# Kernel tuning notes

Hardware: AMD Instinct MI355X
Metric: run time of the kernel (lower is better)

## Reference

```python
import jax, jax.numpy as jnp
import numpy as np

IN_FEATURES = 4096
OUT_FEATURES = 4096
GROUP_SIZE = 128
PACKED_COLS = IN_FEATURES // 8
GROUP_COUNT = IN_FEATURES // GROUP_SIZE


def setup_inputs() -> dict:
    key = jax.random.key(0)
    k1, k2, k3, k4 = jax.random.split(key, 4)
    x = jax.random.normal(k1, (4, 2048, IN_FEATURES), dtype=jnp.float32)
    # packed int4 weights: 8 nibbles per int32 word
    qweight = jax.random.randint(k2, (OUT_FEATURES, PACKED_COLS), jnp.iinfo(jnp.int32).min, jnp.iinfo(jnp.int32).max, dtype=jnp.int32)
    qscale = (jax.random.uniform(k3, (GROUP_COUNT, OUT_FEATURES), dtype=jnp.float32) + 0.5) * 0.01
    qzeros = jax.random.randint(k4, (GROUP_COUNT, OUT_FEATURES), 0, 16, dtype=jnp.int32)
    return {"x": x, "qweight": qweight, "qscale": qscale, "qzeros": qzeros}


def _dequantize(qweight, qscale, qzeros):
    out_f, packed_cols = qweight.shape
    in_f = packed_cols * 8
    shifts = jnp.arange(0, 32, 4, dtype=jnp.int32)  # 8 nibbles per int32
    # (out, packed, 8) -> (out, in)
    w_int = ((qweight[:, :, None] >> shifts) & 15).reshape(out_f, in_f).astype(jnp.float32)
    w_int = w_int[:, :IN_FEATURES]
    gids = jnp.arange(IN_FEATURES, dtype=jnp.int32) // GROUP_SIZE  # (in,)
    scales = qscale[gids].T   # (out, in)
    zeros = qzeros[gids].astype(jnp.float32).T  # (out, in)
    return (w_int - zeros) * scales


def reference(x, qweight, qscale, qzeros):
    w = _dequantize(qweight, qscale, qzeros).astype(jnp.bfloat16)  # compute_dtype
    y = jnp.einsum('bsi,oi->bso', x.astype(jnp.bfloat16), w)
    return y.astype(x.dtype)
```

## Files before the change

### kernel.cpp

```cpp
#include <hip/hip_runtime.h>
#include <hip/hip_bf16.h>

#define IN_F   4096
#define OUT_F  4096
#define PACKED (IN_F / 8)
#define M_DIM  8192
#define N_DIM  OUT_F
#define K_DIM  IN_F

#define BM 256
#define BN 256
#define BK 64
#define NT (K_DIM / BK)
#define NHALF (4 * NT)

typedef __bf16 bf16x8 __attribute__((ext_vector_type(8)));
typedef float  f32x4  __attribute__((ext_vector_type(4)));

#define BAR() asm volatile("s_barrier" ::: "memory")

__global__ __launch_bounds__(256) void dequant_kernel(
    const int* __restrict__ qw, const float* __restrict__ qs,
    const int* __restrict__ qz, __bf16* __restrict__ W)
{
    int t = blockIdx.x * blockDim.x + threadIdx.x;
    if (t >= OUT_F * PACKED) return;
    int o = t >> 9;
    int c = t & (PACKED - 1);
    int g = c >> 4;
    unsigned int q = (unsigned int)qw[t];
    float scale = qs[g * OUT_F + o];
    float zero  = (float)qz[g * OUT_F + o];
    bf16x8 v;
#pragma unroll
    for (int i = 0; i < 8; ++i) {
        float wi = (float)((q >> (4 * i)) & 15u);
        v[i] = (__bf16)((wi - zero) * scale);
    }
    *reinterpret_cast<bf16x8*>(&W[(size_t)t * 8]) = v;
}

__global__ __launch_bounds__(256) void cvt_kernel(
    const float* __restrict__ x, __bf16* __restrict__ xb, int n8)
{
    int t = blockIdx.x * blockDim.x + threadIdx.x;
    if (t >= n8) return;
    const float4* xv = reinterpret_cast<const float4*>(x);
    float4 a = xv[2 * t];
    float4 b = xv[2 * t + 1];
    bf16x8 v;
    v[0] = (__bf16)a.x; v[1] = (__bf16)a.y; v[2] = (__bf16)a.z; v[3] = (__bf16)a.w;
    v[4] = (__bf16)b.x; v[5] = (__bf16)b.y; v[6] = (__bf16)b.z; v[7] = (__bf16)b.w;
    reinterpret_cast<bf16x8*>(xb)[t] = v;
}

__global__ __launch_bounds__(512, 2) void gemm_kernel(
    const __bf16* __restrict__ A, const __bf16* __restrict__ B,
    float* __restrict__ C)
{
    extern __shared__ __bf16 lds[];

    const int tid  = threadIdx.x;
    const int lane = tid & 63;
    const int wave = tid >> 6;
    const int wm   = wave >> 2;
    const int wn   = wave & 3;

    const int bid = blockIdx.x;
    const int swz = (bid & 7) * 64 + (bid >> 3);
    const int nBase = (swz & 15) * BN;
    const int mBase = (swz >> 4) * BM;

    const int lr = lane & 15;
    const int lk = (lane >> 4) * 8;

    auto stage_half = [&](const __bf16* __restrict__ src, __bf16* dstMat,
                          int rowBase, int k0, int hh) {
#pragma unroll
        for (int i = 0; i < 2; ++i) {
            const int st = hh * 16 + i * 8 + wave;
            const int r  = (st >> 1) * 16 + lr;
            const int c  = (st & 1) * 32 + lk;
            __builtin_amdgcn_global_load_lds(
                (const __attribute__((address_space(1))) void*)(src + (size_t)(rowBase + r) * K_DIM + (k0 + c)),
                (__attribute__((address_space(3))) void*)(dstMat + st * 512 + lane * 8), 16, 0, 0);
        }
    };
    auto stage_H = [&](int H) {
        const int t = H >> 2;
        const int h = H & 3;
        __bf16* base = lds + (size_t)(t & 1) * 32768 + (size_t)(h >> 1) * 16384;
        if (h & 2) stage_half(B, base, nBase, t * BK, h & 1);
        else       stage_half(A, base, mBase, t * BK, h & 1);
    };

    f32x4 acc[8][4];
#pragma unroll
    for (int i = 0; i < 8; ++i)
#pragma unroll
        for (int j = 0; j < 4; ++j)
            acc[i][j] = 0.0f;

#pragma unroll
    for (int H = 0; H < 7; ++H) stage_H(H);
    asm volatile("s_waitcnt vmcnt(6)" ::: "memory");
    BAR();

#define LDA(mi, kb) (*(const bf16x8*)(lA + (((wm * 8 + (mi)) * 2 + (kb)) * 512 + lane * 8)))
#define LDB(ni, kb) (*(const bf16x8*)(lB + (((wn * 4 + (ni)) * 2 + (kb)) * 512 + lane * 8)))

    for (int t = 0; t < NT; ++t) {
        const __bf16* lA = lds + (size_t)(t & 1) * 32768;
        const __bf16* lB = lA + 16384;
        const int Hb = 4 * t + 7;
        bf16x8 Af[8][2];
        bf16x8 Bf[2][2];

#pragma unroll
        for (int mi = 0; mi < 4; ++mi) { Af[mi][0] = LDA(mi, 0); Af[mi][1] = LDA(mi, 1); }
#pragma unroll
        for (int ni = 0; ni < 2; ++ni) { Bf[ni][0] = LDB(ni, 0); Bf[ni][1] = LDB(ni, 1); }
        __builtin_amdgcn_sched_barrier(0);
        if (Hb < NHALF) stage_H(Hb);
        BAR();
        __builtin_amdgcn_s_setprio(1);
#pragma unroll
        for (int kb = 0; kb < 2; ++kb)
#pragma unroll
            for (int mi = 0; mi < 4; ++mi)
#pragma unroll
                for (int ni = 0; ni < 2; ++ni)
                    acc[mi][ni] = __builtin_amdgcn_mfma_f32_16x16x32_bf16(Af[mi][kb], Bf[ni][kb], acc[mi][ni], 0, 0, 0);
        __builtin_amdgcn_s_setprio(0);
        BAR();

#pragma unroll
        for (int mi = 4; mi < 8; ++mi) { Af[mi][0] = LDA(mi, 0); Af[mi][1] = LDA(mi, 1); }
        __builtin_amdgcn_sched_barrier(0);
        if (Hb + 1 < NHALF) stage_H(Hb + 1);
        BAR();
        __builtin_amdgcn_s_setprio(1);
#pragma unroll
        for (int kb = 0; kb < 2; ++kb)
#pragma unroll
            for (int mi = 4; mi < 8; ++mi)
#pragma unroll
                for (int ni = 0; ni < 2; ++ni)
                    acc[mi][ni] = __builtin_amdgcn_mfma_f32_16x16x32_bf16(Af[mi][kb], Bf[ni][kb], acc[mi][ni], 0, 0, 0);
        __builtin_amdgcn_s_setprio(0);
        BAR();

#pragma unroll
        for (int ni = 0; ni < 2; ++ni) { Bf[ni][0] = LDB(ni + 2, 0); Bf[ni][1] = LDB(ni + 2, 1); }
        __builtin_amdgcn_sched_barrier(0);
        if (Hb + 2 < NHALF) stage_H(Hb + 2);
        BAR();
        __builtin_amdgcn_s_setprio(1);
#pragma unroll
        for (int kb = 0; kb < 2; ++kb)
#pragma unroll
            for (int mi = 0; mi < 4; ++mi)
#pragma unroll
                for (int nj = 0; nj < 2; ++nj)
                    acc[mi][nj + 2] = __builtin_amdgcn_mfma_f32_16x16x32_bf16(Af[mi][kb], Bf[nj][kb], acc[mi][nj + 2], 0, 0, 0);
        __builtin_amdgcn_s_setprio(0);
        BAR();

        if (Hb + 3 < NHALF) stage_H(Hb + 3);
        BAR();
        __builtin_amdgcn_s_setprio(1);
#pragma unroll
        for (int kb = 0; kb < 2; ++kb)
#pragma unroll
            for (int mi = 4; mi < 8; ++mi)
#pragma unroll
                for (int nj = 0; nj < 2; ++nj)
                    acc[mi][nj + 2] = __builtin_amdgcn_mfma_f32_16x16x32_bf16(Af[mi][kb], Bf[nj][kb], acc[mi][nj + 2], 0, 0, 0);
        __builtin_amdgcn_s_setprio(0);
        if (t < NT - 2)       asm volatile("s_waitcnt vmcnt(6)" ::: "memory");
        else if (t == NT - 2) asm volatile("s_waitcnt vmcnt(0)" ::: "memory");
        BAR();
    }

#pragma unroll
    for (int mi = 0; mi < 8; ++mi)
#pragma unroll
        for (int ni = 0; ni < 4; ++ni) {
            const int col = nBase + wn * 64 + ni * 16 + lr;
#pragma unroll
            for (int r = 0; r < 4; ++r) {
                const int row = mBase + wm * 128 + mi * 16 + (lane >> 4) * 4 + r;
                C[(size_t)row * N_DIM + col] = (float)(__bf16)acc[mi][ni][r];
            }
        }
#undef LDA
#undef LDB
}

extern "C" void kernel_launch(void* const* d_in, const int* in_sizes, int n_in,
                              void* d_out, int out_size, void* d_ws, size_t ws_size,
                              hipStream_t stream)
{
    const float* x       = (const float*)d_in[0];
    const int*   qweight = (const int*)d_in[1];
    const float* qscale  = (const float*)d_in[2];
    const int*   qzeros  = (const int*)d_in[3];
    float*       out     = (float*)d_out;

    __bf16* W  = (__bf16*)d_ws;
    __bf16* xb = (__bf16*)((char*)d_ws + (size_t)N_DIM * K_DIM * sizeof(__bf16));

    {
        int total = OUT_F * PACKED;
        dequant_kernel<<<(total + 255) / 256, 256, 0, stream>>>(qweight, qscale, qzeros, W);
    }
    {
        int n8 = (M_DIM * K_DIM) / 8;
        cvt_kernel<<<(n8 + 255) / 256, 256, 0, stream>>>(x, xb, n8);
    }
    {
        (void)hipFuncSetAttribute((const void*)gemm_kernel,
                                  hipFuncAttributeMaxDynamicSharedMemorySize, 131072);
        dim3 grid((M_DIM / BM) * (N_DIM / BN));
        gemm_kernel<<<grid, 512, 131072, stream>>>(xb, W, out);
    }
}
```

Baseline: 303.5 us.

## Restructure GEMM main loop into two-tile unrolled ping-pong with register-fragment prefetch

Rewrites the GEMM main loop to handle two K-tiles per iteration. A and B fragments are prefetched from LDS into separate register sets one quadrant ahead, so each MFMA phase overlaps the LDS read for the next phase. The issue order of global-to-LDS loads and the vmcnt waits are rescheduled to match the new quadrant order. This is meant to hide LDS read latency behind MFMA work, at the cost of more vector registers live at once, which risks spills or lower occupancy under launch_bounds(512,2).

```diff
diff --git a/kernel.cpp b/kernel.cpp
--- a/kernel.cpp
+++ b/kernel.cpp
@@ -5,19 +5,19 @@
 #define OUT_F  4096
 #define PACKED (IN_F / 8)
 #define M_DIM  8192
-#define N_DIM  OUT_F
-#define K_DIM  IN_F
+#define N_DIM  4096
+#define K_DIM  4096
 
 #define BM 256
 #define BN 256
 #define BK 64
 #define NT (K_DIM / BK)
-#define NHALF (4 * NT)
 
 typedef __bf16 bf16x8 __attribute__((ext_vector_type(8)));
 typedef float  f32x4  __attribute__((ext_vector_type(4)));
 
 #define BAR() asm volatile("s_barrier" ::: "memory")
+#define VMCNT(n) asm volatile("s_waitcnt vmcnt(" #n ")" ::: "memory")
 
 __global__ __launch_bounds__(256) void dequant_kernel(
     const int* __restrict__ qw, const float* __restrict__ qs,
@@ -54,6 +54,41 @@
     reinterpret_cast<bf16x8*>(xb)[t] = v;
 }
 
+__device__ __forceinline__ void read_A4(bf16x8 (&dst)[4][2], const __bf16* base,
+                                        int rb0, int lane8)
+{
+#pragma unroll
+    for (int mi = 0; mi < 4; ++mi)
+#pragma unroll
+        for (int kb = 0; kb < 2; ++kb)
+            dst[mi][kb] = *reinterpret_cast<const bf16x8*>(
+                base + (((rb0 + mi) * 2 + kb) * 512 + lane8));
+}
+
+__device__ __forceinline__ void read_B2(bf16x8 (&dst)[2][2], const __bf16* base,
+                                        int rb0, int lane8)
+{
+#pragma unroll
+    for (int ni = 0; ni < 2; ++ni)
+#pragma unroll
+        for (int kb = 0; kb < 2; ++kb)
+            dst[ni][kb] = *reinterpret_cast<const bf16x8*>(
+                base + (((rb0 + ni) * 2 + kb) * 512 + lane8));
+}
+
+__device__ __forceinline__ void mfma_q(f32x4 (&acc)[8][4], const bf16x8 (&A)[4][2],
+                                       const bf16x8 (&B)[2][2], int r0, int c0)
+{
+#pragma unroll
+    for (int kb = 0; kb < 2; ++kb)
+#pragma unroll
+        for (int mi = 0; mi < 4; ++mi)
+#pragma unroll
+            for (int ni = 0; ni < 2; ++ni)
+                acc[r0 + mi][c0 + ni] = __builtin_amdgcn_mfma_f32_16x16x32_bf16(
+                    A[mi][kb], B[ni][kb], acc[r0 + mi][c0 + ni], 0, 0, 0);
+}
+
 __global__ __launch_bounds__(512, 2) void gemm_kernel(
     const __bf16* __restrict__ A, const __bf16* __restrict__ B,
     float* __restrict__ C)
@@ -65,6 +100,9 @@
     const int wave = tid >> 6;
     const int wm   = wave >> 2;
     const int wn   = wave & 3;
+    const int wm8  = wm * 8;
+    const int wn4  = wn * 4;
+    const int lane8 = lane * 8;
 
     const int bid = blockIdx.x;
     const int swz = (bid & 7) * 64 + (bid >> 3);
@@ -73,6 +111,11 @@
 
     const int lr = lane & 15;
     const int lk = (lane >> 4) * 8;
+
+    __bf16* bufA0 = lds;
+    __bf16* bufB0 = lds + 16384;
+    __bf16* bufA1 = lds + 32768;
+    __bf16* bufB1 = lds + 49152;
 
     auto stage_half = [&](const __bf16* __restrict__ src, __bf16* dstMat,
                           int rowBase, int k0, int hh) {
@@ -86,13 +129,6 @@
                 (__attribute__((address_space(3))) void*)(dstMat + st * 512 + lane * 8), 16, 0, 0);
         }
     };
-    auto stage_H = [&](int H) {
-        const int t = H >> 2;
-        const int h = H & 3;
-        __bf16* base = lds + (size_t)(t & 1) * 32768 + (size_t)(h >> 1) * 16384;
-        if (h & 2) stage_half(B, base, nBase, t * BK, h & 1);
-        else       stage_half(A, base, mBase, t * BK, h & 1);
-    };
 
     f32x4 acc[8][4];
 #pragma unroll
@@ -101,84 +137,100 @@
         for (int j = 0; j < 4; ++j)
             acc[i][j] = 0.0f;
 
-#pragma unroll
-    for (int H = 0; H < 7; ++H) stage_H(H);
-    asm volatile("s_waitcnt vmcnt(6)" ::: "memory");
+    bf16x8 fA03a[4][2], fA03b[4][2], fA47[4][2];
+    bf16x8 fB01a[2][2], fB01b[2][2], fB23[2][2];
+
+    stage_half(A, bufA0, mBase, 0, 0);
+    stage_half(A, bufA0, mBase, 0, 1);
+    stage_half(B, bufB0, nBase, 0, 0);
+    stage_half(B, bufB0, nBase, 0, 1);
+    stage_half(A, bufA1, mBase, BK, 0);
+    stage_half(A, bufA1, mBase, BK, 1);
+    VMCNT(4);
     BAR();
-
-#define LDA(mi, kb) (*(const bf16x8*)(lA + (((wm * 8 + (mi)) * 2 + (kb)) * 512 + lane * 8)))
-#define LDB(ni, kb) (*(const bf16x8*)(lB + (((wn * 4 + (ni)) * 2 + (kb)) * 512 + lane * 8)))
-
-    for (int t = 0; t < NT; ++t) {
-        const __bf16* lA = lds + (size_t)(t & 1) * 32768;
-        const __bf16* lB = lA + 16384;
-        const int Hb = 4 * t + 7;
-        bf16x8 Af[8][2];
-        bf16x8 Bf[2][2];
-
-#pragma unroll
-        for (int mi = 0; mi < 4; ++mi) { Af[mi][0] = LDA(mi, 0); Af[mi][1] = LDA(mi, 1); }
-#pragma unroll
-        for (int ni = 0; ni < 2; ++ni) { Bf[ni][0] = LDB(ni, 0); Bf[ni][1] = LDB(ni, 1); }
-        __builtin_amdgcn_sched_barrier(0);
-        if (Hb < NHALF) stage_H(Hb);
-        BAR();
-        __builtin_amdgcn_s_setprio(1);
-#pragma unroll
-        for (int kb = 0; kb < 2; ++kb)
-#pragma unroll
-            for (int mi = 0; mi < 4; ++mi)
-#pragma unroll
-                for (int ni = 0; ni < 2; ++ni)
-                    acc[mi][ni] = __builtin_amdgcn_mfma_f32_16x16x32_bf16(Af[mi][kb], Bf[ni][kb], acc[mi][ni], 0, 0, 0);
-        __builtin_amdgcn_s_setprio(0);
-        BAR();
-
-#pragma unroll
-        for (int mi = 4; mi < 8; ++mi) { Af[mi][0] = LDA(mi, 0); Af[mi][1] = LDA(mi, 1); }
-        __builtin_amdgcn_sched_barrier(0);
-        if (Hb + 1 < NHALF) stage_H(Hb + 1);
-        BAR();
-        __builtin_amdgcn_s_setprio(1);
-#pragma unroll
-        for (int kb = 0; kb < 2; ++kb)
-#pragma unroll
-            for (int mi = 4; mi < 8; ++mi)
-#pragma unroll
-                for (int ni = 0; ni < 2; ++ni)
-                    acc[mi][ni] = __builtin_amdgcn_mfma_f32_16x16x32_bf16(Af[mi][kb], Bf[ni][kb], acc[mi][ni], 0, 0, 0);
-        __builtin_amdgcn_s_setprio(0);
-        BAR();
-
-#pragma unroll
-        for (int ni = 0; ni < 2; ++ni) { Bf[ni][0] = LDB(ni + 2, 0); Bf[ni][1] = LDB(ni + 2, 1); }
-        __builtin_amdgcn_sched_barrier(0);
-        if (Hb + 2 < NHALF) stage_H(Hb + 2);
-        BAR();
-        __builtin_amdgcn_s_setprio(1);
-#pragma unroll
-        for (int kb = 0; kb < 2; ++kb)
-#pragma unroll
-            for (int mi = 0; mi < 4; ++mi)
-#pragma unroll
-                for (int nj = 0; nj < 2; ++nj)
-                    acc[mi][nj + 2] = __builtin_amdgcn_mfma_f32_16x16x32_bf16(Af[mi][kb], Bf[nj][kb], acc[mi][nj + 2], 0, 0, 0);
-        __builtin_amdgcn_s_setprio(0);
-        BAR();
-
-        if (Hb + 3 < NHALF) stage_H(Hb + 3);
-        BAR();
-        __builtin_amdgcn_s_setprio(1);
-#pragma unroll
-        for (int kb = 0; kb < 2; ++kb)
-#pragma unroll
-            for (int mi = 4; mi < 8; ++mi)
-#pragma unroll
-                for (int nj = 0; nj < 2; ++nj)
-                    acc[mi][nj + 2] = __builtin_amdgcn_mfma_f32_16x16x32_bf16(Af[mi][kb], Bf[nj][kb], acc[mi][nj + 2], 0, 0, 0);
-        __builtin_amdgcn_s_setprio(0);
-        if (t < NT - 2)       asm volatile("s_waitcnt vmcnt(6)" ::: "memory");
-        else if (t == NT - 2) asm volatile("s_waitcnt vmcnt(0)" ::: "memory");
+    read_A4(fA03a, bufA0, wm8 + 0, lane8);
+    read_B2(fB01a, bufB0, wn4 + 0, lane8);
+
+    for (int i2 = 0; i2 < NT / 2; ++i2) {
+        const int te = 2 * i2;
+        const bool sA_e = (te + 2) < NT;
+        const bool sO   = (te + 2) < NT;
+        const bool sA_o = (te + 3) < NT;
+
+        read_B2(fB23, bufB0, wn4 + 2, lane8);
+        __builtin_amdgcn_sched_barrier(0);
+        stage_half(B, bufB1, nBase, (te + 1) * BK, 0);
+        BAR();
+        __builtin_amdgcn_s_setprio(1);
+        mfma_q(acc, fA03a, fB01a, 0, 0);
+        __builtin_amdgcn_s_setprio(0);
+        BAR();
+
+        read_A4(fA47, bufA0, wm8 + 4, lane8);
+        __builtin_amdgcn_sched_barrier(0);
+        stage_half(B, bufB1, nBase, (te + 1) * BK, 1);
+        BAR();
+        __builtin_amdgcn_s_setprio(1);
+        mfma_q(acc, fA03a, fB23, 0, 2);
+        __builtin_amdgcn_s_setprio(0);
+        VMCNT(4);
+        BAR();
+
+        read_A4(fA03b, bufA1, wm8 + 0, lane8);
+        __builtin_amdgcn_sched_barrier(0);
+        if (sA_e) stage_half(A, bufA0, mBase, (te + 2) * BK, 0);
+        BAR();
+        __builtin_amdgcn_s_setprio(1);
+        mfma_q(acc, fA47, fB23, 4, 2);
+        __builtin_amdgcn_s_setprio(0);
+        if (sA_e) { VMCNT(2); } else { VMCNT(0); }
+        BAR();
+
+        read_B2(fB01b, bufB1, wn4 + 0, lane8);
+        __builtin_amdgcn_sched_barrier(0);
+        if (sA_e) stage_half(A, bufA0, mBase, (te + 2) * BK, 1);
+        BAR();
+        __builtin_amdgcn_s_setprio(1);
+        mfma_q(acc, fA47, fB01a, 4, 0);
+        __builtin_amdgcn_s_setprio(0);
+        BAR();
+
+        read_B2(fB23, bufB1, wn4 + 2, lane8);
+        __builtin_amdgcn_sched_barrier(0);
+        if (sO) stage_half(B, bufB0, nBase, (te + 2) * BK, 0);
+        BAR();
+        __builtin_amdgcn_s_setprio(1);
+        mfma_q(acc, fA03b, fB01b, 0, 0);
+        __builtin_amdgcn_s_setprio(0);
+        BAR();
+
+        read_A4(fA47, bufA1, wm8 + 4, lane8);
+        __builtin_amdgcn_sched_barrier(0);
+        if (sO) stage_half(B, bufB0, nBase, (te + 2) * BK, 1);
+        BAR();
+        __builtin_amdgcn_s_setprio(1);
+        mfma_q(acc, fA03b, fB23, 0, 2);
+        __builtin_amdgcn_s_setprio(0);
+        VMCNT(4);
+        BAR();
+
+        read_A4(fA03a, bufA0, wm8 + 0, lane8);
+        __builtin_amdgcn_sched_barrier(0);
+        if (sA_o) stage_half(A, bufA1, mBase, (te + 3) * BK, 0);
+        BAR();
+        __builtin_amdgcn_s_setprio(1);
+        mfma_q(acc, fA47, fB23, 4, 2);
+        __builtin_amdgcn_s_setprio(0);
+        if (sA_o) { VMCNT(2); } else { VMCNT(0); }
+        BAR();
+
+        read_B2(fB01a, bufB0, wn4 + 0, lane8);
+        __builtin_amdgcn_sched_barrier(0);
+        if (sA_o) stage_half(A, bufA1, mBase, (te + 3) * BK, 1);
+        BAR();
+        __builtin_amdgcn_s_setprio(1);
+        mfma_q(acc, fA47, fB01b, 4, 0);
+        __builtin_amdgcn_s_setprio(0);
         BAR();
     }
 
@@ -193,8 +245,6 @@
                 C[(size_t)row * N_DIM + col] = (float)(__bf16)acc[mi][ni][r];
             }
         }
-#undef LDA
-#undef LDB
 }
 
 extern "C" void kernel_launch(void* const* d_in, const int* in_sizes, int n_in,
```

Result: slower. 697.5 us (+129.8%).

## Pre-tile bf16 operands into LDS-fragment order so GEMM staging reads contiguous chunks

Applied to the files above, without the earlier changes.

The dequant and convert kernels now write W and x in a blocked layout that matches the GEMM's LDS fragment order (128-row halves by 64-wide k-tiles). Each 8 KB staging slice then becomes one contiguous global block instead of 16-byte pieces strided across rows. This is meant to improve coalescing and cut address arithmetic in the GEMM's global_load_lds staging. In exchange, the producer kernels compute scattered gather addresses for their reads; the convert kernel now reads 32-byte chunks from different rows, which may lower read efficiency on the large x tensor.

```diff
diff --git a/kernel.cpp b/kernel.cpp
--- a/kernel.cpp
+++ b/kernel.cpp
@@ -5,8 +5,8 @@
 #define OUT_F  4096
 #define PACKED (IN_F / 8)
 #define M_DIM  8192
-#define N_DIM  OUT_F
-#define K_DIM  IN_F
+#define N_DIM  4096
+#define K_DIM  4096
 
 #define BM 256
 #define BN 256
@@ -18,17 +18,23 @@
 typedef float  f32x4  __attribute__((ext_vector_type(4)));
 
 #define BAR() asm volatile("s_barrier" ::: "memory")
+#define VMCNT(n) asm volatile("s_waitcnt vmcnt(" #n ")" ::: "memory")
+
 
 __global__ __launch_bounds__(256) void dequant_kernel(
     const int* __restrict__ qw, const float* __restrict__ qs,
     const int* __restrict__ qz, __bf16* __restrict__ W)
 {
-    int t = blockIdx.x * blockDim.x + threadIdx.x;
-    if (t >= OUT_F * PACKED) return;
-    int o = t >> 9;
-    int c = t & (PACKED - 1);
-    int g = c >> 4;
-    unsigned int q = (unsigned int)qw[t];
+    int ch = blockIdx.x * blockDim.x + threadIdx.x;
+    if (ch >= OUT_F * PACKED) return;
+    int l     = ch & 63;
+    int st    = (ch >> 6) & 15;
+    int kTile = (ch >> 10) & 63;
+    int nHalf = ch >> 16;
+    int o  = nHalf * 128 + ((st >> 1) << 4) + (l & 15);
+    int k0 = kTile * 64 + ((st & 1) << 5) + ((l >> 4) << 3);
+    int g  = k0 >> 7;
+    unsigned int q = (unsigned int)qw[o * PACKED + (k0 >> 3)];
     float scale = qs[g * OUT_F + o];
     float zero  = (float)qz[g * OUT_F + o];
     bf16x8 v;
@@ -37,21 +43,27 @@
         float wi = (float)((q >> (4 * i)) & 15u);
         v[i] = (__bf16)((wi - zero) * scale);
     }
-    *reinterpret_cast<bf16x8*>(&W[(size_t)t * 8]) = v;
+    *reinterpret_cast<bf16x8*>(&W[(size_t)ch * 8]) = v;
 }
 
 __global__ __launch_bounds__(256) void cvt_kernel(
-    const float* __restrict__ x, __bf16* __restrict__ xb, int n8)
-{
-    int t = blockIdx.x * blockDim.x + threadIdx.x;
-    if (t >= n8) return;
-    const float4* xv = reinterpret_cast<const float4*>(x);
-    float4 a = xv[2 * t];
-    float4 b = xv[2 * t + 1];
+    const float* __restrict__ x, __bf16* __restrict__ xb, int nch)
+{
+    int ch = blockIdx.x * blockDim.x + threadIdx.x;
+    if (ch >= nch) return;
+    int l     = ch & 63;
+    int st    = (ch >> 6) & 15;
+    int kTile = (ch >> 10) & 63;
+    int mHalf = ch >> 16;
+    int m  = mHalf * 128 + ((st >> 1) << 4) + (l & 15);
+    int k0 = kTile * 64 + ((st & 1) << 5) + ((l >> 4) << 3);
+    const float4* xv = reinterpret_cast<const float4*>(x + (size_t)m * K_DIM + k0);
+    float4 a = xv[0];
+    float4 b = xv[1];
     bf16x8 v;
     v[0] = (__bf16)a.x; v[1] = (__bf16)a.y; v[2] = (__bf16)a.z; v[3] = (__bf16)a.w;
     v[4] = (__bf16)b.x; v[5] = (__bf16)b.y; v[6] = (__bf16)b.z; v[7] = (__bf16)b.w;
-    reinterpret_cast<bf16x8*>(xb)[t] = v;
+    reinterpret_cast<bf16x8*>(xb)[ch] = v;
 }
 
 __global__ __launch_bounds__(512, 2) void gemm_kernel(
@@ -70,28 +82,29 @@
     const int swz = (bid & 7) * 64 + (bid >> 3);
     const int nBase = (swz & 15) * BN;
     const int mBase = (swz >> 4) * BM;
+    const int mHalf0 = mBase >> 7;
+    const int nHalf0 = nBase >> 7;
 
     const int lr = lane & 15;
-    const int lk = (lane >> 4) * 8;
-
-    auto stage_half = [&](const __bf16* __restrict__ src, __bf16* dstMat,
-                          int rowBase, int k0, int hh) {
+
+    auto stage_half = [&](const __bf16* __restrict__ srcFrag, __bf16* dstMat,
+                          int halfGlobal, int kTile, int hh) {
+        const __bf16* base = srcFrag + ((size_t)(halfGlobal * 64 + kTile) << 13);
 #pragma unroll
         for (int i = 0; i < 2; ++i) {
-            const int st = hh * 16 + i * 8 + wave;
-            const int r  = (st >> 1) * 16 + lr;
-            const int c  = (st & 1) * 32 + lk;
+            const int st = i * 8 + wave;
             __builtin_amdgcn_global_load_lds(
-                (const __attribute__((address_space(1))) void*)(src + (size_t)(rowBase + r) * K_DIM + (k0 + c)),
-                (__attribute__((address_space(3))) void*)(dstMat + st * 512 + lane * 8), 16, 0, 0);
+                (const __attribute__((address_space(1))) void*)(base + st * 512 + lane * 8),
+                (__attribute__((address_space(3))) void*)(dstMat + (hh * 16 + st) * 512 + lane * 8),
+                16, 0, 0);
         }
     };
     auto stage_H = [&](int H) {
         const int t = H >> 2;
         const int h = H & 3;
         __bf16* base = lds + (size_t)(t & 1) * 32768 + (size_t)(h >> 1) * 16384;
-        if (h & 2) stage_half(B, base, nBase, t * BK, h & 1);
-        else       stage_half(A, base, mBase, t * BK, h & 1);
+        if (h & 2) stage_half(B, base, nHalf0 + (h & 1), t, h & 1);
+        else       stage_half(A, base, mHalf0 + (h & 1), t, h & 1);
     };
 
     f32x4 acc[8][4];
@@ -103,7 +116,7 @@
 
 #pragma unroll
     for (int H = 0; H < 7; ++H) stage_H(H);
-    asm volatile("s_waitcnt vmcnt(6)" ::: "memory");
+    VMCNT(6);
     BAR();
 
 #define LDA(mi, kb) (*(const bf16x8*)(lA + (((wm * 8 + (mi)) * 2 + (kb)) * 512 + lane * 8)))
@@ -177,8 +190,8 @@
                 for (int nj = 0; nj < 2; ++nj)
                     acc[mi][nj + 2] = __builtin_amdgcn_mfma_f32_16x16x32_bf16(Af[mi][kb], Bf[nj][kb], acc[mi][nj + 2], 0, 0, 0);
         __builtin_amdgcn_s_setprio(0);
-        if (t < NT - 2)       asm volatile("s_waitcnt vmcnt(6)" ::: "memory");
-        else if (t == NT - 2) asm volatile("s_waitcnt vmcnt(0)" ::: "memory");
+        if (t < NT - 2)       VMCNT(6);
+        else if (t == NT - 2) VMCNT(0);
         BAR();
     }
 
@@ -215,8 +228,8 @@
         dequant_kernel<<<(total + 255) / 256, 256, 0, stream>>>(qweight, qscale, qzeros, W);
     }
     {
-        int n8 = (M_DIM * K_DIM) / 8;
-        cvt_kernel<<<(n8 + 255) / 256, 256, 0, stream>>>(x, xb, n8);
+        int nch = (M_DIM * K_DIM) / 8;
+        cvt_kernel<<<(nch + 255) / 256, 256, 0, stream>>>(x, xb, nch);
     }
     {
         (void)hipFuncSetAttribute((const void*)gemm_kernel,
```

After: 276.7 us. 1.1x faster.
